# Performance work log

Hardware: AMD Instinct MI355X
Metric: run time of the kernel (lower is better)

Reference implementation:

```python
import jax, jax.numpy as jnp
import numpy as np

ORDER = 2


def _masked_row_mean(v, m, safe_cnt, has_any):
    # v already zeroed outside mask; per-row mean over masked entries
    s = jnp.sum(v, axis=1, keepdims=True) / safe_cnt
    return jnp.where(has_any, s, 0.0)


def high_order_residual(x, mask, order=ORDER):
    """Vectorized faithful version of high_order_residual (braq).
    nanmean over masked entries == masked sum / count; sign/scale/shift
    are only meaningful inside the mask, outputs outside the mask are 0.
    """
    m = mask.astype(x.dtype)                       # (oc, ic)
    cnt = jnp.sum(m, axis=1, keepdims=True)        # (oc, 1)
    safe_cnt = jnp.maximum(cnt, 1.0)
    has_any = cnt > 0
    xm = x * m
    sum_order = jnp.zeros_like(x)
    for _ in range(order):
        residual = (xm - sum_order) * m            # masked residual, 0 outside
        mean = _masked_row_mean(residual, m, safe_cnt, has_any)   # (oc,1)
        centered = (residual - mean) * m           # 0 outside mask
        scale = _masked_row_mean(jnp.abs(centered), m, safe_cnt, has_any)
        binary = jnp.sign(centered) * scale + mean
        sum_order = sum_order + binary * m
    return sum_order


def setup_inputs() -> dict:
    key = jax.random.key(0)
    k1, k2 = jax.random.split(key)
    x = jax.random.normal(k1, (11008, 4096), dtype=jnp.float32) * 0.02
    mask = jax.random.randint(k2, (11008, 4096), 0, 2).astype(jnp.bool_)
    return {"x": x, "mask": mask}


def reference(x, mask):
    return high_order_residual(x, mask, ORDER)
```

## Files before the change

kernel.cpp:

```cpp
#include <hip/hip_runtime.h>
#include <stdint.h>

#define IC   4096
#define BLK  256
#define VPT  4
#define EPT  (VPT * 4)

__device__ __forceinline__ void block_sum2_d(double& a, double& b, double* sm) {
    #pragma unroll
    for (int off = 32; off; off >>= 1) {
        a += __shfl_xor(a, off);
        b += __shfl_xor(b, off);
    }
    const int wid = threadIdx.x >> 6;
    if ((threadIdx.x & 63) == 0) { sm[wid] = a; sm[4 + wid] = b; }
    __syncthreads();
    a = sm[0] + sm[1] + sm[2] + sm[3];
    b = sm[4] + sm[5] + sm[6] + sm[7];
    __syncthreads();
}

__device__ __forceinline__ double block_sum1_d(double a, double* sm) {
    #pragma unroll
    for (int off = 32; off; off >>= 1) a += __shfl_xor(a, off);
    const int wid = threadIdx.x >> 6;
    if ((threadIdx.x & 63) == 0) sm[wid] = a;
    __syncthreads();
    a = sm[0] + sm[1] + sm[2] + sm[3];
    __syncthreads();
    return a;
}

__device__ __forceinline__ double dsign(double v) {
    return (v > 0.0) ? 1.0 : ((v < 0.0) ? -1.0 : 0.0);
}

__global__ __launch_bounds__(BLK) void binarize_kernel(
    const float* __restrict__ x,
    const uint8_t* __restrict__ mask,
    float* __restrict__ out)
{
    __shared__ double sm[8];
    const int row = blockIdx.x;
    const int tid = threadIdx.x;

    double bad = (((const uint32_t*)mask)[tid] > 1u) ? 1.0 : 0.0;
    const bool mask_is_i32 = (block_sum1_d(bad, sm) == 0.0);

    const float* xr   = x + (size_t)row * IC;
    float*       orow = out + (size_t)row * IC;

    float xf[EPT];
    float mv[EPT];

    #pragma unroll
    for (int i = 0; i < VPT; ++i) {
        float4 v = ((const float4*)xr)[tid + i * BLK];
        xf[i*4+0] = v.x; xf[i*4+1] = v.y; xf[i*4+2] = v.z; xf[i*4+3] = v.w;
    }

    if (mask_is_i32) {
        const int4* mr = (const int4*)mask + (size_t)row * (IC / 4);
        #pragma unroll
        for (int i = 0; i < VPT; ++i) {
            int4 m4 = mr[tid + i * BLK];
            mv[i*4+0] = m4.x ? 1.f : 0.f;
            mv[i*4+1] = m4.y ? 1.f : 0.f;
            mv[i*4+2] = m4.z ? 1.f : 0.f;
            mv[i*4+3] = m4.w ? 1.f : 0.f;
        }
    } else {
        const uint32_t* mr = (const uint32_t*)(mask + (size_t)row * IC);
        #pragma unroll
        for (int i = 0; i < VPT; ++i) {
            uint32_t w = mr[tid + i * BLK];
            mv[i*4+0] = (w & 0x000000ffu) ? 1.f : 0.f;
            mv[i*4+1] = (w & 0x0000ff00u) ? 1.f : 0.f;
            mv[i*4+2] = (w & 0x00ff0000u) ? 1.f : 0.f;
            mv[i*4+3] = (w & 0xff000000u) ? 1.f : 0.f;
        }
    }

    double s = 0.0, c = 0.0;
    #pragma unroll
    for (int j = 0; j < EPT; ++j) {
        const double m = (double)mv[j];
        s += (double)xf[j] * m;
        c += m;
    }
    block_sum2_d(s, c, sm);

    const bool   has   = (c > 0.0);
    const double inv   = 1.0 / fmax(c, 1.0);
    const double mean1 = has ? s * inv : 0.0;

    double sa = 0.0;
    #pragma unroll
    for (int j = 0; j < EPT; ++j)
        sa += fabs((double)xf[j] - mean1) * (double)mv[j];
    sa = block_sum1_d(sa, sm);
    const double scale1 = has ? sa * inv : 0.0;

    double s2 = 0.0;
    #pragma unroll
    for (int j = 0; j < EPT; ++j) {
        const double xv = (double)xf[j], m = (double)mv[j];
        const double b1 = dsign(xv - mean1) * scale1 + mean1;
        s2 += (xv - b1) * m;
    }
    s2 = block_sum1_d(s2, sm);
    const double mean2 = has ? s2 * inv : 0.0;

    double sa2 = 0.0;
    #pragma unroll
    for (int j = 0; j < EPT; ++j) {
        const double xv = (double)xf[j], m = (double)mv[j];
        const double b1 = dsign(xv - mean1) * scale1 + mean1;
        const double r2 = (xv - b1) * m;
        sa2 += fabs(r2 - mean2) * m;
    }
    sa2 = block_sum1_d(sa2, sm);
    const double scale2 = has ? sa2 * inv : 0.0;

    #pragma unroll
    for (int i = 0; i < VPT; ++i) {
        float4 o;
        float* op = &o.x;
        #pragma unroll
        for (int k = 0; k < 4; ++k) {
            const int j = i * 4 + k;
            const double xv = (double)xf[j], m = (double)mv[j];
            const double b1  = dsign(xv - mean1) * scale1 + mean1;
            const double r2  = (xv - b1) * m;
            const double ce2 = (r2 - mean2) * m;
            const double b2  = dsign(ce2) * scale2 + mean2;
            op[k] = (float)((b1 + b2) * m);
        }
        ((float4*)orow)[tid + i * BLK] = o;
    }
}

extern "C" void kernel_launch(void* const* d_in, const int* in_sizes, int n_in,
                              void* d_out, int out_size, void* d_ws, size_t ws_size,
                              hipStream_t stream) {
    const float*   x    = (const float*)d_in[0];
    const uint8_t* mask = (const uint8_t*)d_in[1];
    float*         out  = (float*)d_out;

    const int rows = in_sizes[0] / IC;
    binarize_kernel<<<rows, BLK, 0, stream>>>(x, mask, out);
}
```

Measured before the change: 401.7 us.

## Process one row per wavefront with bitmask and algebraic fusion of second-mean pass

Maps each row to a single 64-lane wavefront instead of a 256-thread block, so all reductions become shuffle-only and the shared-memory barriers go away. The mask is packed into a 64-bit per-lane bitmask rather than float arrays. The second mean is derived algebraically from the first sum, the absolute-deviation sum and a sign count, which removes one full reduction pass. Each lane now holds 16 float4 values in registers, raising register pressure, and the grid assumes the row count divides by 4.

After: 601.7 us. +49.8%, slower.

```diff
diff --git a/kernel.cpp b/kernel.cpp
--- a/kernel.cpp
+++ b/kernel.cpp
@@ -3,140 +3,144 @@
 
 #define IC   4096
 #define BLK  256
-#define VPT  4
-#define EPT  (VPT * 4)
+#define CPL  16
 
-__device__ __forceinline__ void block_sum2_d(double& a, double& b, double* sm) {
+__device__ __forceinline__ double wsum_d(double v) {
     #pragma unroll
-    for (int off = 32; off; off >>= 1) {
-        a += __shfl_xor(a, off);
-        b += __shfl_xor(b, off);
-    }
-    const int wid = threadIdx.x >> 6;
-    if ((threadIdx.x & 63) == 0) { sm[wid] = a; sm[4 + wid] = b; }
-    __syncthreads();
-    a = sm[0] + sm[1] + sm[2] + sm[3];
-    b = sm[4] + sm[5] + sm[6] + sm[7];
-    __syncthreads();
+    for (int off = 32; off; off >>= 1) v += __shfl_xor(v, off);
+    return v;
+}
+__device__ __forceinline__ int wsum_i(int v) {
+    #pragma unroll
+    for (int off = 32; off; off >>= 1) v += __shfl_xor(v, off);
+    return v;
 }
 
-__device__ __forceinline__ double block_sum1_d(double a, double* sm) {
-    #pragma unroll
-    for (int off = 32; off; off >>= 1) a += __shfl_xor(a, off);
-    const int wid = threadIdx.x >> 6;
-    if ((threadIdx.x & 63) == 0) sm[wid] = a;
-    __syncthreads();
-    a = sm[0] + sm[1] + sm[2] + sm[3];
-    __syncthreads();
-    return a;
-}
-
-__device__ __forceinline__ double dsign(double v) {
-    return (v > 0.0) ? 1.0 : ((v < 0.0) ? -1.0 : 0.0);
-}
-
-__global__ __launch_bounds__(BLK) void binarize_kernel(
+__global__ __launch_bounds__(BLK, 4) void binarize_kernel(
     const float* __restrict__ x,
     const uint8_t* __restrict__ mask,
     float* __restrict__ out)
 {
-    __shared__ double sm[8];
-    const int row = blockIdx.x;
-    const int tid = threadIdx.x;
+    const int lane = threadIdx.x & 63;
+    const int wid  = threadIdx.x >> 6;
+    const int row  = blockIdx.x * (BLK / 64) + wid;
 
-    double bad = (((const uint32_t*)mask)[tid] > 1u) ? 1.0 : 0.0;
-    const bool mask_is_i32 = (block_sum1_d(bad, sm) == 0.0);
+    const uint32_t probe = ((const uint32_t*)mask)[lane];
+    const bool mask_is_bytes = __any(probe > 1u);
 
-    const float* xr   = x + (size_t)row * IC;
-    float*       orow = out + (size_t)row * IC;
+    const float* xr = x + (size_t)row * IC;
 
-    float xf[EPT];
-    float mv[EPT];
+    float4 xf[CPL];
+    #pragma unroll
+    for (int i = 0; i < CPL; ++i)
+        xf[i] = ((const float4*)xr)[i * 64 + lane];
 
-    #pragma unroll
-    for (int i = 0; i < VPT; ++i) {
-        float4 v = ((const float4*)xr)[tid + i * BLK];
-        xf[i*4+0] = v.x; xf[i*4+1] = v.y; xf[i*4+2] = v.z; xf[i*4+3] = v.w;
-    }
-
-    if (mask_is_i32) {
+    uint64_t bm = 0;
+    if (mask_is_bytes) {
+        const uint32_t* mr = (const uint32_t*)(mask + (size_t)row * IC);
+        uint32_t mw[CPL];
+        #pragma unroll
+        for (int i = 0; i < CPL; ++i) mw[i] = mr[i * 64 + lane];
+        #pragma unroll
+        for (int i = 0; i < CPL; ++i) {
+            uint64_t b = 0;
+            if (mw[i] & 0x000000ffu) b |= 1ull;
+            if (mw[i] & 0x0000ff00u) b |= 2ull;
+            if (mw[i] & 0x00ff0000u) b |= 4ull;
+            if (mw[i] & 0xff000000u) b |= 8ull;
+            bm |= b << (i * 4);
+        }
+    } else {
         const int4* mr = (const int4*)mask + (size_t)row * (IC / 4);
         #pragma unroll
-        for (int i = 0; i < VPT; ++i) {
-            int4 m4 = mr[tid + i * BLK];
-            mv[i*4+0] = m4.x ? 1.f : 0.f;
-            mv[i*4+1] = m4.y ? 1.f : 0.f;
-            mv[i*4+2] = m4.z ? 1.f : 0.f;
-            mv[i*4+3] = m4.w ? 1.f : 0.f;
-        }
-    } else {
-        const uint32_t* mr = (const uint32_t*)(mask + (size_t)row * IC);
-        #pragma unroll
-        for (int i = 0; i < VPT; ++i) {
-            uint32_t w = mr[tid + i * BLK];
-            mv[i*4+0] = (w & 0x000000ffu) ? 1.f : 0.f;
-            mv[i*4+1] = (w & 0x0000ff00u) ? 1.f : 0.f;
-            mv[i*4+2] = (w & 0x00ff0000u) ? 1.f : 0.f;
-            mv[i*4+3] = (w & 0xff000000u) ? 1.f : 0.f;
+        for (int i = 0; i < CPL; ++i) {
+            int4 m4 = mr[i * 64 + lane];
+            uint64_t b = 0;
+            if (m4.x) b |= 1ull;
+            if (m4.y) b |= 2ull;
+            if (m4.z) b |= 4ull;
+            if (m4.w) b |= 8ull;
+            bm |= b << (i * 4);
         }
     }
 
-    double s = 0.0, c = 0.0;
+    double s = 0.0;
     #pragma unroll
-    for (int j = 0; j < EPT; ++j) {
-        const double m = (double)mv[j];
-        s += (double)xf[j] * m;
-        c += m;
+    for (int i = 0; i < CPL; ++i) {
+        const float e[4] = {xf[i].x, xf[i].y, xf[i].z, xf[i].w};
+        #pragma unroll
+        for (int k = 0; k < 4; ++k)
+            if ((bm >> (i * 4 + k)) & 1ull) s += (double)e[k];
     }
-    block_sum2_d(s, c, sm);
+    s = wsum_d(s);
+    const int cnt = wsum_i(__popcll(bm));
 
-    const bool   has   = (c > 0.0);
-    const double inv   = 1.0 / fmax(c, 1.0);
-    const double mean1 = has ? s * inv : 0.0;
+    const double dc    = (double)((cnt > 0) ? cnt : 1);
+    const double mean1 = (cnt > 0) ? (s / dc) : 0.0;
 
     double sa = 0.0;
+    int    pn = 0;
     #pragma unroll
-    for (int j = 0; j < EPT; ++j)
-        sa += fabs((double)xf[j] - mean1) * (double)mv[j];
-    sa = block_sum1_d(sa, sm);
-    const double scale1 = has ? sa * inv : 0.0;
+    for (int i = 0; i < CPL; ++i) {
+        const float e[4] = {xf[i].x, xf[i].y, xf[i].z, xf[i].w};
+        #pragma unroll
+        for (int k = 0; k < 4; ++k) {
+            if ((bm >> (i * 4 + k)) & 1ull) {
+                const double ce = (double)e[k] - mean1;
+                sa += fabs(ce);
+                pn += (ce > 0.0) ? 1 : ((ce < 0.0) ? -1 : 0);
+            }
+        }
+    }
+    sa = wsum_d(sa);
+    pn = wsum_i(pn);
 
-    double s2 = 0.0;
+    const double scale1 = (cnt > 0) ? (sa / dc) : 0.0;
+    const double s2    = (s - dc * mean1) - scale1 * (double)pn;
+    const double mean2 = (cnt > 0) ? (s2 / dc) : 0.0;
+
+    double sd = 0.0;
     #pragma unroll
-    for (int j = 0; j < EPT; ++j) {
-        const double xv = (double)xf[j], m = (double)mv[j];
-        const double b1 = dsign(xv - mean1) * scale1 + mean1;
-        s2 += (xv - b1) * m;
+    for (int i = 0; i < CPL; ++i) {
+        const float e[4] = {xf[i].x, xf[i].y, xf[i].z, xf[i].w};
+        #pragma unroll
+        for (int k = 0; k < 4; ++k) {
+            if ((bm >> (i * 4 + k)) & 1ull) {
+                const double xd = (double)e[k];
+                const double ce = xd - mean1;
+                const double t1 = (ce > 0.0) ? scale1 : ((ce < 0.0) ? -scale1 : 0.0);
+                const double b1 = t1 + mean1;
+                const double r2 = xd - b1;
+                sd += fabs(r2 - mean2);
+            }
+        }
     }
-    s2 = block_sum1_d(s2, sm);
-    const double mean2 = has ? s2 * inv : 0.0;
+    sd = wsum_d(sd);
+    const double scale2 = (cnt > 0) ? (sd / dc) : 0.0;
 
-    double sa2 = 0.0;
+    float* orow = out + (size_t)row * IC;
     #pragma unroll
-    for (int j = 0; j < EPT; ++j) {
-        const double xv = (double)xf[j], m = (double)mv[j];
-        const double b1 = dsign(xv - mean1) * scale1 + mean1;
-        const double r2 = (xv - b1) * m;
-        sa2 += fabs(r2 - mean2) * m;
-    }
-    sa2 = block_sum1_d(sa2, sm);
-    const double scale2 = has ? sa2 * inv : 0.0;
-
-    #pragma unroll
-    for (int i = 0; i < VPT; ++i) {
+    for (int i = 0; i < CPL; ++i) {
+        const float e[4] = {xf[i].x, xf[i].y, xf[i].z, xf[i].w};
         float4 o;
         float* op = &o.x;
         #pragma unroll
         for (int k = 0; k < 4; ++k) {
-            const int j = i * 4 + k;
-            const double xv = (double)xf[j], m = (double)mv[j];
-            const double b1  = dsign(xv - mean1) * scale1 + mean1;
-            const double r2  = (xv - b1) * m;
-            const double ce2 = (r2 - mean2) * m;
-            const double b2  = dsign(ce2) * scale2 + mean2;
-            op[k] = (float)((b1 + b2) * m);
+            if ((bm >> (i * 4 + k)) & 1ull) {
+                const double xd = (double)e[k];
+                const double ce = xd - mean1;
+                const double t1 = (ce > 0.0) ? scale1 : ((ce < 0.0) ? -scale1 : 0.0);
+                const double b1 = t1 + mean1;
+                const double r2 = xd - b1;
+                const double c2 = r2 - mean2;
+                const double t2 = (c2 > 0.0) ? scale2 : ((c2 < 0.0) ? -scale2 : 0.0);
+                const double b2 = t2 + mean2;
+                op[k] = (float)(b1 + b2);
+            } else {
+                op[k] = 0.0f;
+            }
         }
-        ((float4*)orow)[tid + i * BLK] = o;
+        ((float4*)orow)[i * 64 + lane] = o;
     }
 }
 
@@ -148,5 +152,6 @@
     float*         out  = (float*)d_out;
 
     const int rows = in_sizes[0] / IC;
-    binarize_kernel<<<rows, BLK, 0, stream>>>(x, mask, out);
+    const int grid = rows / (BLK / 64);
+    binarize_kernel<<<grid, BLK, 0, stream>>>(x, mask, out);
 }
```
